# Kernel tuning notes

Measured on AMD Instinct MI355X. Metric: run time of the kernel, lower is better.

Reference implementation:

```python
import jax, jax.numpy as jnp
import numpy as np
import math

D_MODEL = 256
N_HEADS = 8
N_LEVELS = 4
N_POINTS = 4
D_HEAD = D_MODEL // N_HEADS
SPATIAL_SHAPES = np.array([[64, 64], [32, 32], [16, 16], [8, 8]], dtype=np.int64)


def _offset_bias():
    # faithful to MSDeformAttn._reset_parameters grid init for sampling_offsets bias
    thetas = np.arange(N_HEADS, dtype=np.float32) * (2.0 * math.pi / N_HEADS)
    grid = np.stack([np.cos(thetas), np.sin(thetas)], -1)
    grid = grid / np.abs(grid).max(-1, keepdims=True)
    grid = np.tile(grid[:, None, None, :], (1, N_LEVELS, N_POINTS, 1)).copy()
    for i in range(N_POINTS):
        grid[:, :, i, :] *= i + 1
    return jnp.asarray(grid.reshape(-1), jnp.float32)


def setup_inputs() -> dict:
    key = jax.random.key(0)
    ks = jax.random.split(key, 8)
    N, Q = 2, 10000
    areas = SPATIAL_SHAPES[:, 0] * SPATIAL_SHAPES[:, 1]
    len_in = int(areas.sum())
    lsi = np.concatenate([[0], np.cumsum(areas)[:-1]])
    s = 1.0 / float(np.sqrt(D_MODEL))
    return {
        "query": jax.random.normal(ks[0], (N, Q, D_MODEL), jnp.float32),
        "reference_points": jax.random.uniform(ks[1], (N, Q, N_LEVELS, 2), jnp.float32),
        "input_flatten": jax.random.normal(ks[2], (N, len_in, D_MODEL), jnp.float32),
        "input_spatial_shapes": jnp.asarray(SPATIAL_SHAPES, jnp.int32),
        "input_level_start_index": jnp.asarray(lsi, jnp.int32),
        "W_value": jax.random.normal(ks[3], (D_MODEL, D_MODEL), jnp.float32) * s,
        "b_value": jnp.zeros((D_MODEL,), jnp.float32),
        "W_off": jax.random.normal(ks[4], (D_MODEL, N_HEADS * N_LEVELS * N_POINTS * 2), jnp.float32) * 0.01,
        "b_off": _offset_bias(),
        "W_attn": jax.random.normal(ks[5], (D_MODEL, N_HEADS * N_LEVELS * N_POINTS), jnp.float32) * 0.01,
        "b_attn": jnp.zeros((N_HEADS * N_LEVELS * N_POINTS,), jnp.float32),
        "W_out": jax.random.normal(ks[6], (D_MODEL, D_MODEL), jnp.float32) * s,
        "b_out": jnp.zeros((D_MODEL,), jnp.float32),
    }


def _bilinear(val, loc, H, W):
    # val: (B, H*W, d); loc: (B, S, 2) in [0,1]; matches F.grid_sample(align_corners=False, padding_mode='zeros')
    x = loc[..., 0] * W - 0.5
    y = loc[..., 1] * H - 0.5
    x0f = jnp.floor(x)
    y0f = jnp.floor(y)
    wx = (x - x0f)[..., None]
    wy = (y - y0f)[..., None]
    x0 = x0f.astype(jnp.int32)
    y0 = y0f.astype(jnp.int32)

    def gather(xi, yi):
        valid = ((xi >= 0) & (xi < W) & (yi >= 0) & (yi < H))[..., None]
        idx = jnp.clip(yi, 0, H - 1) * W + jnp.clip(xi, 0, W - 1)
        return jnp.take_along_axis(val, idx[..., None], axis=1) * valid

    v00 = gather(x0, y0)
    v01 = gather(x0 + 1, y0)
    v10 = gather(x0, y0 + 1)
    v11 = gather(x0 + 1, y0 + 1)
    return v00 * (1 - wx) * (1 - wy) + v01 * wx * (1 - wy) + v10 * (1 - wx) * wy + v11 * wx * wy


def _forward(query, reference_points, input_flatten, W_value, b_value, W_off, b_off, W_attn, b_attn, W_out, b_out):
    N, Q, _ = query.shape
    value = (input_flatten @ W_value + b_value).reshape(N, -1, N_HEADS, D_HEAD)
    off = (query @ W_off + b_off).reshape(N, Q, N_HEADS, N_LEVELS, N_POINTS, 2)
    attn = jax.nn.softmax((query @ W_attn + b_attn).reshape(N, Q, N_HEADS, N_LEVELS * N_POINTS), axis=-1)
    attn = attn.reshape(N, Q, N_HEADS, N_LEVELS, N_POINTS)
    # offset normalizer is (W_l, H_l) per level
    norm = jnp.asarray(np.stack([SPATIAL_SHAPES[:, 1], SPATIAL_SHAPES[:, 0]], -1), query.dtype)
    loc = reference_points[:, :, None, :, None, :] + off / norm[None, None, None, :, None, :]
    start = 0
    sampled = []
    for l in range(N_LEVELS):
        H_, W_ = int(SPATIAL_SHAPES[l, 0]), int(SPATIAL_SHAPES[l, 1])
        val_l = value[:, start:start + H_ * W_]  # (N, HW, nH, d)
        val_l = val_l.transpose(0, 2, 1, 3).reshape(N * N_HEADS, H_ * W_, D_HEAD)
        loc_l = loc[:, :, :, l].transpose(0, 2, 1, 3, 4).reshape(N * N_HEADS, Q * N_POINTS, 2)
        s_l = _bilinear(val_l, loc_l, H_, W_).reshape(N, N_HEADS, Q, N_POINTS, D_HEAD)
        sampled.append(s_l)
        start += H_ * W_
    sampled = jnp.stack(sampled, axis=3)  # (N, nH, Q, L, P, d)
    out = jnp.einsum('nhqlpd,nqhlp->nqhd', sampled, attn).reshape(N, Q, D_MODEL)
    return out @ W_out + b_out


def reference(query, reference_points, input_flatten, input_spatial_shapes, input_level_start_index, W_value, b_value, W_off, b_off, W_attn, b_attn, W_out, b_out):
    # input_spatial_shapes / input_level_start_index are static metadata (SPATIAL_SHAPES)
    return _forward(query, reference_points, input_flatten, W_value, b_value, W_off, b_off, W_attn, b_attn, W_out, b_out)
```

## Files before the change

kernel.cpp:

```cpp
#include <hip/hip_runtime.h>

#define NB 2
#define NQ 10000
#define DM 256
#define NHEADS 8
#define NLEV 4
#define NPTS 4
#define DHEAD 32
#define LEN_IN 5440

typedef _Float16 f16x8 __attribute__((ext_vector_type(8)));
typedef _Float16 f16x4 __attribute__((ext_vector_type(4)));
typedef float    f32x4 __attribute__((ext_vector_type(4)));
typedef unsigned short u16x4 __attribute__((ext_vector_type(4)));

union TaskU {
    struct { f16x4 w; u16x4 p; } s;
    uint4 u;
};

__device__ __forceinline__ void swz_one(const float* __restrict__ W, int Nw,
                                        int srcCol, int kbase,
                                        _Float16* __restrict__ dst) {
    f16x8 v;
    #pragma unroll
    for (int j = 0; j < 8; ++j) v[j] = (_Float16)W[(size_t)(kbase + j) * Nw + srcCol];
    *(f16x8*)dst = v;
}

__global__ __launch_bounds__(256) void prep(const float* __restrict__ Wv,
                                            const float* __restrict__ Wo,
                                            const float* __restrict__ Wa,
                                            const float* __restrict__ Wout,
                                            const float* __restrict__ query,
                                            const float* __restrict__ inflat,
                                            _Float16* __restrict__ Wv_swz,
                                            _Float16* __restrict__ Wofa_swz,
                                            _Float16* __restrict__ Wout_swz,
                                            _Float16* __restrict__ query_h,
                                            _Float16* __restrict__ inflat_h) {
    const int b = blockIdx.x;
    const int t = threadIdx.x;
    if (b < 112) {
        const int tid = b * 256 + t;
        if (tid < 8192) {
            const int lane = tid & 63, tt = tid >> 6, kt = tt & 7, nt = tt >> 3;
            swz_one(Wv, 256, nt * 16 + (lane & 15), kt * 32 + (lane >> 4) * 8,
                    Wv_swz + ((size_t)(nt * 8 + kt) * 64 + lane) * 8);
        } else if (tid < 16384) {
            const int local = tid - 8192;
            const int lane = local & 63, tt = local >> 6, kt = tt & 7, nt = tt >> 3;
            swz_one(Wo, 256, nt * 16 + (lane & 15), kt * 32 + (lane >> 4) * 8,
                    Wofa_swz + ((size_t)(nt * 8 + kt) * 64 + lane) * 8);
        } else if (tid < 20480) {
            const int local = tid - 16384;
            const int lane = local & 63, tt = local >> 6, kt = tt & 7, nt = tt >> 3;
            swz_one(Wa, 128, nt * 16 + (lane & 15), kt * 32 + (lane >> 4) * 8,
                    Wofa_swz + ((size_t)((16 + nt) * 8 + kt) * 64 + lane) * 8);
        } else if (tid < 28672) {
            const int local = tid - 20480;
            const int lane = local & 63, tt = local >> 6, kt = tt & 7, nt = tt >> 3;
            swz_one(Wout, 256, nt * 16 + (lane & 15), kt * 32 + (lane >> 4) * 8,
                    Wout_swz + ((size_t)(nt * 8 + kt) * 64 + lane) * 8);
        }
    } else if (b < 112 + 2500) {
        const size_t e = ((size_t)(b - 112) * 256 + t) * 8;
        const float4 lo = *(const float4*)(query + e);
        const float4 hi = *(const float4*)(query + e + 4);
        f16x8 o;
        o[0] = (_Float16)lo.x; o[1] = (_Float16)lo.y; o[2] = (_Float16)lo.z; o[3] = (_Float16)lo.w;
        o[4] = (_Float16)hi.x; o[5] = (_Float16)hi.y; o[6] = (_Float16)hi.z; o[7] = (_Float16)hi.w;
        *(f16x8*)(query_h + e) = o;
    } else {
        const size_t e = ((size_t)(b - 2612) * 256 + t) * 8;
        const float4 lo = *(const float4*)(inflat + e);
        const float4 hi = *(const float4*)(inflat + e + 4);
        f16x8 o;
        o[0] = (_Float16)lo.x; o[1] = (_Float16)lo.y; o[2] = (_Float16)lo.z; o[3] = (_Float16)lo.w;
        o[4] = (_Float16)hi.x; o[5] = (_Float16)hi.y; o[6] = (_Float16)hi.z; o[7] = (_Float16)hi.w;
        *(f16x8*)(inflat_h + e) = o;
    }
}

template<int OUTMODE>
__device__ __forceinline__ void tile_gemm(const _Float16* __restrict__ A,
                                          const _Float16* __restrict__ Wswz,
                                          const float* __restrict__ bias0,
                                          const float* __restrict__ bias1,
                                          int bsplit,
                                          void* __restrict__ C_,
                                          int M, int N, int mb, int nb) {
    const int lane = threadIdx.x & 63;
    const int w = threadIdx.x >> 6;
    const int wm = w & 1, wn = w >> 1;
    const int m0 = mb + wm * 32;
    const int n0 = nb + wn * 32;
    const int r = lane & 15;
    const int klane = (lane >> 4) * 8;
    const int rc0 = min(m0 + r, M - 1);
    const int rc1 = min(m0 + 16 + r, M - 1);
    const int ntile0 = n0 >> 4;

    f32x4 acc[2][2] = {};
    #pragma unroll
    for (int kt = 0; kt < 8; ++kt) {
        const f16x8 a0 = *(const f16x8*)(A + (size_t)rc0 * 256 + kt * 32 + klane);
        const f16x8 a1 = *(const f16x8*)(A + (size_t)rc1 * 256 + kt * 32 + klane);
        const f16x8 b0 = *(const f16x8*)(Wswz + ((size_t)((ntile0 + 0) * 8 + kt) * 64 + lane) * 8);
        const f16x8 b1 = *(const f16x8*)(Wswz + ((size_t)((ntile0 + 1) * 8 + kt) * 64 + lane) * 8);
        acc[0][0] = __builtin_amdgcn_mfma_f32_16x16x32_f16(a0, b0, acc[0][0], 0, 0, 0);
        acc[0][1] = __builtin_amdgcn_mfma_f32_16x16x32_f16(a0, b1, acc[0][1], 0, 0, 0);
        acc[1][0] = __builtin_amdgcn_mfma_f32_16x16x32_f16(a1, b0, acc[1][0], 0, 0, 0);
        acc[1][1] = __builtin_amdgcn_mfma_f32_16x16x32_f16(a1, b1, acc[1][1], 0, 0, 0);
    }
    #pragma unroll
    for (int j = 0; j < 2; ++j) {
        const int col = n0 + j * 16 + r;
        const float bb = (col < bsplit) ? bias0[col] : bias1[col - bsplit];
        #pragma unroll
        for (int i = 0; i < 2; ++i) {
            #pragma unroll
            for (int rr = 0; rr < 4; ++rr) {
                const int row = m0 + i * 16 + (lane >> 4) * 4 + rr;
                if (row < M) {
                    const float v = acc[i][j][rr] + bb;
                    if constexpr (OUTMODE == 0) {
                        ((_Float16*)C_)[(size_t)row * N + col] = (_Float16)v;
                    } else if constexpr (OUTMODE == 1) {
                        ((float*)C_)[(size_t)row * N + col] = v;
                    } else {
                        const int n_img = row >= LEN_IN;
                        const int pix = row - (n_img ? LEN_IN : 0);
                        ((_Float16*)C_)[((((size_t)(n_img * 8 + (col >> 5)) * LEN_IN) + pix) << 5)
                                        + (col & 31)] = (_Float16)v;
                    }
                }
            }
        }
    }
}

__global__ __launch_bounds__(256) void gemm_front(const _Float16* __restrict__ inflat_h,
                                                  const _Float16* __restrict__ query_h,
                                                  const _Float16* __restrict__ Wv_swz,
                                                  const _Float16* __restrict__ Wofa_swz,
                                                  const float* __restrict__ b_value,
                                                  const float* __restrict__ b_off,
                                                  const float* __restrict__ b_attn,
                                                  _Float16* __restrict__ value_h,
                                                  _Float16* __restrict__ ofa_h) {
    const int bx = blockIdx.x;
    if (bx < 680) {
        tile_gemm<2>(inflat_h, Wv_swz, b_value, b_value, 256, value_h,
                     NB * LEN_IN, 256, (bx % 170) * 64, (bx / 170) * 64);
    } else {
        const int b2 = bx - 680;
        tile_gemm<0>(query_h, Wofa_swz, b_off, b_attn, 256, ofa_h,
                     NB * NQ, 384, (b2 % 313) * 64, (b2 / 313) * 64);
    }
}

__global__ __launch_bounds__(256) void gemm_out(const _Float16* __restrict__ A,
                                                const _Float16* __restrict__ Wswz,
                                                const float* __restrict__ bias,
                                                float* __restrict__ C, int M) {
    tile_gemm<1>(A, Wswz, bias, bias, 256, C, M, 256,
                 blockIdx.x * 64, blockIdx.y * 64);
}

__device__ __forceinline__ f16x8 sp8(_Float16 w) {
    return (f16x8){w, w, w, w, w, w, w, w};
}

__global__ __launch_bounds__(256) void sample_kernel(const float* __restrict__ refp,
                                                     const _Float16* __restrict__ ofa,
                                                     const _Float16* __restrict__ value,
                                                     _Float16* __restrict__ out_pre) {
    __shared__ float attns_s[8][128];
    __shared__ float refs[8][NLEV][2];
    __shared__ uint4 tasks[1024];

    const int t = threadIdx.x;
    const int blk = blockIdx.x;
    const int n = blk / (NQ / 8);
    const int q0 = (blk % (NQ / 8)) * 8;
    const size_t qb = (size_t)n * NQ + q0;

    if (t < 64) {
        {
            const int i = t >> 3, rem = t & 7;
            refs[i][rem >> 1][rem & 1] = refp[(qb + i) * NLEV * 2 + rem];
        }
        const int q = t >> 3, h = t & 7;
        const _Float16* arow = ofa + (qb + q) * 384 + 256 + h * 16;
        const f16x8 a0 = *(const f16x8*)arow;
        const f16x8 a1 = *(const f16x8*)(arow + 8);
        float a[16];
        #pragma unroll
        for (int j = 0; j < 8; ++j) { a[j] = (float)a0[j]; a[8 + j] = (float)a1[j]; }
        float m = a[0];
        #pragma unroll
        for (int j = 1; j < 16; ++j) m = fmaxf(m, a[j]);
        float s = 0.f;
        #pragma unroll
        for (int j = 0; j < 16; ++j) { const float e = __expf(a[j] - m); a[j] = e; s += e; }
        const float inv = 1.0f / s;
        #pragma unroll
        for (int j = 0; j < 16; ++j) attns_s[q][h * 16 + j] = a[j] * inv;
    }
    __syncthreads();

    {
        const int q = t >> 5, h = (t >> 2) & 7, lvl = t & 3, qh = t >> 2;
        constexpr int HS[4] = {64, 32, 16, 8};
        constexpr int ST[4] = {0, 4096, 5120, 5376};
        const int H_ = HS[lvl], W_ = HS[lvl], st = ST[lvl];
        const float fW = (float)W_, fH = (float)H_;
        const float invW = 1.0f / fW, invH = 1.0f / fH;
        const float rx = refs[q][lvl][0];
        const float ry = refs[q][lvl][1];
        const f16x8 off8 = *(const f16x8*)(ofa + (qb + q) * 384 + (h * 16 + lvl * 4) * 2);
        const f32x4 at4 = *(const f32x4*)&attns_s[q][h * 16 + lvl * 4];
        #pragma unroll
        for (int pt = 0; pt < NPTS; ++pt) {
            const float lx = rx + (float)off8[pt * 2]     * invW;
            const float ly = ry + (float)off8[pt * 2 + 1] * invH;
            const float aw = at4[pt];
            const float x = lx * fW - 0.5f;
            const float y = ly * fH - 0.5f;
            const float x0f = floorf(x);
            const float y0f = floorf(y);
            const float wx = x - x0f;
            const float wy = y - y0f;
            const int x0 = (int)x0f, y0 = (int)y0f;
            const int x1 = x0 + 1, y1 = y0 + 1;
            const int xc0 = min(max(x0, 0), W_ - 1);
            const int xc1 = min(max(x1, 0), W_ - 1);
            const int yc0 = min(max(y0, 0), H_ - 1);
            const int yc1 = min(max(y1, 0), H_ - 1);
            const bool vx0 = (x0 >= 0) & (x0 < W_);
            const bool vx1 = (x1 >= 0) & (x1 < W_);
            const bool vy0 = (y0 >= 0) & (y0 < H_);
            const bool vy1 = (y1 >= 0) & (y1 < H_);
            const float w00 = (vx0 & vy0) ? aw * (1.f - wx) * (1.f - wy) : 0.f;
            const float w01 = (vx1 & vy0) ? aw * wx         * (1.f - wy) : 0.f;
            const float w10 = (vx0 & vy1) ? aw * (1.f - wx) * wy         : 0.f;
            const float w11 = (vx1 & vy1) ? aw * wx         * wy         : 0.f;
            TaskU tu;
            tu.s.w = (f16x4){(_Float16)w00, (_Float16)w01, (_Float16)w10, (_Float16)w11};
            tu.s.p = (u16x4){(unsigned short)(st + yc0 * W_ + xc0),
                             (unsigned short)(st + yc0 * W_ + xc1),
                             (unsigned short)(st + yc1 * W_ + xc0),
                             (unsigned short)(st + yc1 * W_ + xc1)};
            tasks[qh * 16 + ((lvl * 4 + pt) ^ (qh & 15))] = tu.u;
        }
    }
    __syncthreads();

    {
        const int q = t >> 5, h = (t >> 2) & 7, g = t & 3, qh = t >> 2;
        const _Float16* vhead = value + ((size_t)(n * 8 + h) * LEN_IN) * 32 + g * 8;
        f16x8 acc = {};
        #pragma unroll 4
        for (int ptIdx = 0; ptIdx < 16; ++ptIdx) {
            TaskU tu;
            tu.u = tasks[qh * 16 + (ptIdx ^ (qh & 15))];
            const f16x8 v0 = *(const f16x8*)(vhead + ((size_t)tu.s.p[0] << 5));
            const f16x8 v1 = *(const f16x8*)(vhead + ((size_t)tu.s.p[1] << 5));
            const f16x8 v2 = *(const f16x8*)(vhead + ((size_t)tu.s.p[2] << 5));
            const f16x8 v3 = *(const f16x8*)(vhead + ((size_t)tu.s.p[3] << 5));
            acc += v0 * sp8(tu.s.w[0]);
            acc += v1 * sp8(tu.s.w[1]);
            acc += v2 * sp8(tu.s.w[2]);
            acc += v3 * sp8(tu.s.w[3]);
        }
        *(f16x8*)(out_pre + (qb + q) * DM + h * 32 + g * 8) = acc;
    }
}

extern "C" void kernel_launch(void* const* d_in, const int* in_sizes, int n_in,
                              void* d_out, int out_size, void* d_ws, size_t ws_size,
                              hipStream_t stream) {
    const float* query  = (const float*)d_in[0];
    const float* refp   = (const float*)d_in[1];
    const float* inflat = (const float*)d_in[2];
    const float* W_value = (const float*)d_in[5];
    const float* b_value = (const float*)d_in[6];
    const float* W_off   = (const float*)d_in[7];
    const float* b_off   = (const float*)d_in[8];
    const float* W_attn  = (const float*)d_in[9];
    const float* b_attn  = (const float*)d_in[10];
    const float* W_out   = (const float*)d_in[11];
    const float* b_out   = (const float*)d_in[12];
    float* out = (float*)d_out;

    char* ws = (char*)d_ws;
    _Float16* value_h   = (_Float16*)(ws);
    _Float16* ofa_h     = (_Float16*)(ws + 5570560);
    _Float16* out_pre_h = (_Float16*)(ws + 20930560);
    _Float16* Wv_swz    = (_Float16*)(ws + 20930560);
    _Float16* Wofa_swz  = (_Float16*)(ws + 21061632);
    _Float16* Wout_swz  = (_Float16*)(ws + 31170560);
    _Float16* query_h   = (_Float16*)((char*)d_out);
    _Float16* inflat_h  = (_Float16*)((char*)d_out + 10240000);

    prep<<<3972, 256, 0, stream>>>(W_value, W_off, W_attn, W_out, query, inflat,
                                   Wv_swz, Wofa_swz, Wout_swz, query_h, inflat_h);
    gemm_front<<<2558, 256, 0, stream>>>(inflat_h, query_h, Wv_swz, Wofa_swz,
                                         b_value, b_off, b_attn, value_h, ofa_h);
    sample_kernel<<<2500, 256, 0, stream>>>(refp, ofa_h, value_h, out_pre_h);
    gemm_out<<<dim3(313, 4), 256, 0, stream>>>(out_pre_h, Wout_swz, b_out,
                                               out, NB * NQ);
}
```

Before: 89.70 us.

## Fuse bilinear sampling with output projection GEMM in one kernel

Merges the sampling kernel and the output-projection GEMM into a single kernel. Each block now handles 16 queries in two passes of 8, stages the sampled fp16 rows in swizzled LDS, and then runs a 16x256x256 MFMA projection that reads the pre-swizzled W_out directly from global memory. This drops the out_pre round trip through global memory and one kernel launch. In exchange the block count is halved, each block does more serialized work with extra barriers, and every block re-reads the full W_out.

```diff
diff --git a/kernel.cpp b/kernel.cpp
--- a/kernel.cpp
+++ b/kernel.cpp
@@ -126,8 +126,6 @@
                     const float v = acc[i][j][rr] + bb;
                     if constexpr (OUTMODE == 0) {
                         ((_Float16*)C_)[(size_t)row * N + col] = (_Float16)v;
-                    } else if constexpr (OUTMODE == 1) {
-                        ((float*)C_)[(size_t)row * N + col] = v;
                     } else {
                         const int n_img = row >= LEN_IN;
                         const int pix = row - (n_img ? LEN_IN : 0);
@@ -160,33 +158,28 @@
     }
 }
 
-__global__ __launch_bounds__(256) void gemm_out(const _Float16* __restrict__ A,
-                                                const _Float16* __restrict__ Wswz,
-                                                const float* __restrict__ bias,
-                                                float* __restrict__ C, int M) {
-    tile_gemm<1>(A, Wswz, bias, bias, 256, C, M, 256,
-                 blockIdx.x * 64, blockIdx.y * 64);
-}
-
 __device__ __forceinline__ f16x8 sp8(_Float16 w) {
     return (f16x8){w, w, w, w, w, w, w, w};
 }
 
-__global__ __launch_bounds__(256) void sample_kernel(const float* __restrict__ refp,
-                                                     const _Float16* __restrict__ ofa,
-                                                     const _Float16* __restrict__ value,
-                                                     _Float16* __restrict__ out_pre) {
-    __shared__ float attns_s[8][128];
-    __shared__ float refs[8][NLEV][2];
+__global__ __launch_bounds__(256) void sample_out(const float* __restrict__ refp,
+                                                  const _Float16* __restrict__ ofa,
+                                                  const _Float16* __restrict__ value,
+                                                  const _Float16* __restrict__ Wout_swz,
+                                                  const float* __restrict__ b_out,
+                                                  float* __restrict__ out) {
+    __shared__ float attns_s[16][128];
+    __shared__ float refs[16][NLEV][2];
     __shared__ uint4 tasks[1024];
+    __shared__ uint4 oplds[512];
 
     const int t = threadIdx.x;
     const int blk = blockIdx.x;
-    const int n = blk / (NQ / 8);
-    const int q0 = (blk % (NQ / 8)) * 8;
+    const int n = blk / (NQ / 16);
+    const int q0 = (blk % (NQ / 16)) * 16;
     const size_t qb = (size_t)n * NQ + q0;
 
-    if (t < 64) {
+    if (t < 128) {
         {
             const int i = t >> 3, rem = t & 7;
             refs[i][rem >> 1][rem & 1] = refp[(qb + i) * NLEV * 2 + rem];
@@ -210,71 +203,106 @@
     }
     __syncthreads();
 
+    #pragma unroll 1
+    for (int p = 0; p < 2; ++p) {
+        {
+            const int ql = t >> 5, h = (t >> 2) & 7, lvl = t & 3, qh = t >> 2;
+            const int q = p * 8 + ql;
+            constexpr int HS[4] = {64, 32, 16, 8};
+            constexpr int ST[4] = {0, 4096, 5120, 5376};
+            const int H_ = HS[lvl], W_ = HS[lvl], st = ST[lvl];
+            const float fW = (float)W_, fH = (float)H_;
+            const float invW = 1.0f / fW, invH = 1.0f / fH;
+            const float rx = refs[q][lvl][0];
+            const float ry = refs[q][lvl][1];
+            const f16x8 off8 = *(const f16x8*)(ofa + (qb + q) * 384 + (h * 16 + lvl * 4) * 2);
+            const f32x4 at4 = *(const f32x4*)&attns_s[q][h * 16 + lvl * 4];
+            #pragma unroll
+            for (int pt = 0; pt < NPTS; ++pt) {
+                const float lx = rx + (float)off8[pt * 2]     * invW;
+                const float ly = ry + (float)off8[pt * 2 + 1] * invH;
+                const float aw = at4[pt];
+                const float x = lx * fW - 0.5f;
+                const float y = ly * fH - 0.5f;
+                const float x0f = floorf(x);
+                const float y0f = floorf(y);
+                const float wx = x - x0f;
+                const float wy = y - y0f;
+                const int x0 = (int)x0f, y0 = (int)y0f;
+                const int x1 = x0 + 1, y1 = y0 + 1;
+                const int xc0 = min(max(x0, 0), W_ - 1);
+                const int xc1 = min(max(x1, 0), W_ - 1);
+                const int yc0 = min(max(y0, 0), H_ - 1);
+                const int yc1 = min(max(y1, 0), H_ - 1);
+                const bool vx0 = (x0 >= 0) & (x0 < W_);
+                const bool vx1 = (x1 >= 0) & (x1 < W_);
+                const bool vy0 = (y0 >= 0) & (y0 < H_);
+                const bool vy1 = (y1 >= 0) & (y1 < H_);
+                const float w00 = (vx0 & vy0) ? aw * (1.f - wx) * (1.f - wy) : 0.f;
+                const float w01 = (vx1 & vy0) ? aw * wx         * (1.f - wy) : 0.f;
+                const float w10 = (vx0 & vy1) ? aw * (1.f - wx) * wy         : 0.f;
+                const float w11 = (vx1 & vy1) ? aw * wx         * wy         : 0.f;
+                TaskU tu;
+                tu.s.w = (f16x4){(_Float16)w00, (_Float16)w01, (_Float16)w10, (_Float16)w11};
+                tu.s.p = (u16x4){(unsigned short)(st + yc0 * W_ + xc0),
+                                 (unsigned short)(st + yc0 * W_ + xc1),
+                                 (unsigned short)(st + yc1 * W_ + xc0),
+                                 (unsigned short)(st + yc1 * W_ + xc1)};
+                tasks[qh * 16 + ((lvl * 4 + pt) ^ (qh & 15))] = tu.u;
+            }
+        }
+        __syncthreads();
+        {
+            const int ql = t >> 5, h = (t >> 2) & 7, g = t & 3, qh = t >> 2;
+            const int q = p * 8 + ql;
+            const _Float16* vhead = value + ((size_t)(n * 8 + h) * LEN_IN) * 32 + g * 8;
+            f16x8 acc = {};
+            #pragma unroll 4
+            for (int ptIdx = 0; ptIdx < 16; ++ptIdx) {
+                TaskU tu;
+                tu.u = tasks[qh * 16 + (ptIdx ^ (qh & 15))];
+                const f16x8 v0 = *(const f16x8*)(vhead + ((size_t)tu.s.p[0] << 5));
+                const f16x8 v1 = *(const f16x8*)(vhead + ((size_t)tu.s.p[1] << 5));
+                const f16x8 v2 = *(const f16x8*)(vhead + ((size_t)tu.s.p[2] << 5));
+                const f16x8 v3 = *(const f16x8*)(vhead + ((size_t)tu.s.p[3] << 5));
+                acc += v0 * sp8(tu.s.w[0]);
+                acc += v1 * sp8(tu.s.w[1]);
+                acc += v2 * sp8(tu.s.w[2]);
+                acc += v3 * sp8(tu.s.w[3]);
+            }
+            const int byte = q * 512 + ((h * 64 + g * 16) ^ ((q & 7) << 4));
+            *(f16x8*)((char*)oplds + byte) = acc;
+        }
+        __syncthreads();
+    }
+
     {
-        const int q = t >> 5, h = (t >> 2) & 7, lvl = t & 3, qh = t >> 2;
-        constexpr int HS[4] = {64, 32, 16, 8};
-        constexpr int ST[4] = {0, 4096, 5120, 5376};
-        const int H_ = HS[lvl], W_ = HS[lvl], st = ST[lvl];
-        const float fW = (float)W_, fH = (float)H_;
-        const float invW = 1.0f / fW, invH = 1.0f / fH;
-        const float rx = refs[q][lvl][0];
-        const float ry = refs[q][lvl][1];
-        const f16x8 off8 = *(const f16x8*)(ofa + (qb + q) * 384 + (h * 16 + lvl * 4) * 2);
-        const f32x4 at4 = *(const f32x4*)&attns_s[q][h * 16 + lvl * 4];
-        #pragma unroll
-        for (int pt = 0; pt < NPTS; ++pt) {
-            const float lx = rx + (float)off8[pt * 2]     * invW;
-            const float ly = ry + (float)off8[pt * 2 + 1] * invH;
-            const float aw = at4[pt];
-            const float x = lx * fW - 0.5f;
-            const float y = ly * fH - 0.5f;
-            const float x0f = floorf(x);
-            const float y0f = floorf(y);
-            const float wx = x - x0f;
-            const float wy = y - y0f;
-            const int x0 = (int)x0f, y0 = (int)y0f;
-            const int x1 = x0 + 1, y1 = y0 + 1;
-            const int xc0 = min(max(x0, 0), W_ - 1);
-            const int xc1 = min(max(x1, 0), W_ - 1);
-            const int yc0 = min(max(y0, 0), H_ - 1);
-            const int yc1 = min(max(y1, 0), H_ - 1);
-            const bool vx0 = (x0 >= 0) & (x0 < W_);
-            const bool vx1 = (x1 >= 0) & (x1 < W_);
-            const bool vy0 = (y0 >= 0) & (y0 < H_);
-            const bool vy1 = (y1 >= 0) & (y1 < H_);
-            const float w00 = (vx0 & vy0) ? aw * (1.f - wx) * (1.f - wy) : 0.f;
-            const float w01 = (vx1 & vy0) ? aw * wx         * (1.f - wy) : 0.f;
-            const float w10 = (vx0 & vy1) ? aw * (1.f - wx) * wy         : 0.f;
-            const float w11 = (vx1 & vy1) ? aw * wx         * wy         : 0.f;
-            TaskU tu;
-            tu.s.w = (f16x4){(_Float16)w00, (_Float16)w01, (_Float16)w10, (_Float16)w11};
-            tu.s.p = (u16x4){(unsigned short)(st + yc0 * W_ + xc0),
-                             (unsigned short)(st + yc0 * W_ + xc1),
-                             (unsigned short)(st + yc1 * W_ + xc0),
-                             (unsigned short)(st + yc1 * W_ + xc1)};
-            tasks[qh * 16 + ((lvl * 4 + pt) ^ (qh & 15))] = tu.u;
-        }
-    }
-    __syncthreads();
-
-    {
-        const int q = t >> 5, h = (t >> 2) & 7, g = t & 3, qh = t >> 2;
-        const _Float16* vhead = value + ((size_t)(n * 8 + h) * LEN_IN) * 32 + g * 8;
-        f16x8 acc = {};
-        #pragma unroll 4
-        for (int ptIdx = 0; ptIdx < 16; ++ptIdx) {
-            TaskU tu;
-            tu.u = tasks[qh * 16 + (ptIdx ^ (qh & 15))];
-            const f16x8 v0 = *(const f16x8*)(vhead + ((size_t)tu.s.p[0] << 5));
-            const f16x8 v1 = *(const f16x8*)(vhead + ((size_t)tu.s.p[1] << 5));
-            const f16x8 v2 = *(const f16x8*)(vhead + ((size_t)tu.s.p[2] << 5));
-            const f16x8 v3 = *(const f16x8*)(vhead + ((size_t)tu.s.p[3] << 5));
-            acc += v0 * sp8(tu.s.w[0]);
-            acc += v1 * sp8(tu.s.w[1]);
-            acc += v2 * sp8(tu.s.w[2]);
-            acc += v3 * sp8(tu.s.w[3]);
-        }
-        *(f16x8*)(out_pre + (qb + q) * DM + h * 32 + g * 8) = acc;
+        const int lane = t & 63;
+        const int w = t >> 6;
+        const int r = lane & 15;
+        const int kq = lane >> 4;
+        f32x4 acc[4] = {};
+        #pragma unroll
+        for (int kt = 0; kt < 8; ++kt) {
+            const int abyte = r * 512 + ((kt * 64 + kq * 16) ^ ((r & 7) << 4));
+            const f16x8 a = *(const f16x8*)((const char*)oplds + abyte);
+            #pragma unroll
+            for (int nt = 0; nt < 4; ++nt) {
+                const int ntile = w * 4 + nt;
+                const f16x8 b = *(const f16x8*)(Wout_swz + ((size_t)(ntile * 8 + kt) * 64 + lane) * 8);
+                acc[nt] = __builtin_amdgcn_mfma_f32_16x16x32_f16(a, b, acc[nt], 0, 0, 0);
+            }
+        }
+        #pragma unroll
+        for (int nt = 0; nt < 4; ++nt) {
+            const int col = (w * 4 + nt) * 16 + r;
+            const float bb = b_out[col];
+            #pragma unroll
+            for (int rr = 0; rr < 4; ++rr) {
+                const int row = kq * 4 + rr;
+                out[(qb + row) * 256 + col] = acc[nt][rr] + bb;
+            }
+        }
     }
 }
 
@@ -297,7 +325,6 @@
     char* ws = (char*)d_ws;
     _Float16* value_h   = (_Float16*)(ws);
     _Float16* ofa_h     = (_Float16*)(ws + 5570560);
-    _Float16* out_pre_h = (_Float16*)(ws + 20930560);
     _Float16* Wv_swz    = (_Float16*)(ws + 20930560);
     _Float16* Wofa_swz  = (_Float16*)(ws + 21061632);
     _Float16* Wout_swz  = (_Float16*)(ws + 31170560);
@@ -308,7 +335,6 @@
                                    Wv_swz, Wofa_swz, Wout_swz, query_h, inflat_h);
     gemm_front<<<2558, 256, 0, stream>>>(inflat_h, query_h, Wv_swz, Wofa_swz,
                                          b_value, b_off, b_attn, value_h, ofa_h);
-    sample_kernel<<<2500, 256, 0, stream>>>(refp, ofa_h, value_h, out_pre_h);
-    gemm_out<<<dim3(313, 4), 256, 0, stream>>>(out_pre_h, Wout_swz, b_out,
-                                               out, NB * NQ);
-}
+    sample_out<<<1250, 256, 0, stream>>>(refp, ofa_h, value_h, Wout_swz,
+                                         b_out, out);
+}
```

Result: faster. 81.02 us (-9.7%).
